# Performance work log

Measured on AMD Instinct MI355X. Metric: run time of the kernel, lower is better.

## Reference

```python
import jax, jax.numpy as jnp
import numpy as np

N, D, C, TOPK = 4096, 512, 512, 5


def setup_inputs() -> dict:
    key = jax.random.key(0)
    k1, k2, k3, k4 = jax.random.split(key, 4)
    feat1 = jax.random.normal(k1, (N, D), dtype=jnp.float32)
    feat2 = jax.random.normal(k2, (N, D), dtype=jnp.float32)
    # probs are softmax outputs in the original pipeline -> valid BCE inputs in (0,1)
    prob1 = jax.nn.softmax(jax.random.normal(k3, (N, C), dtype=jnp.float32), axis=-1)
    prob2 = jax.nn.softmax(jax.random.normal(k4, (N, C), dtype=jnp.float32), axis=-1)
    return {"feat1": feat1, "feat2": feat2, "prob1": prob1, "prob2": prob2, "topk": TOPK}


def reference(feat1, feat2, prob1, prob2, topk):
    # rank statistics on detached feat1: top-k feature indices, sorted as a set
    rank_idx = jnp.argsort(-feat1, axis=1)           # descending argsort, (N, D)
    top = jnp.sort(rank_idx[:, :topk], axis=1)       # (N, K) sorted top-k index sets
    # pair_enum layout: pair k = j*N + i with x1 -> row i (fast), x2 -> row j (slow).
    # Build the equivalent (N, N) matrices with rows=j, cols=i.
    rank_diff = jnp.abs(top[None, :, :] - top[:, None, :]).sum(-1)  # (N, N)
    target = (rank_diff == 0).astype(prob1.dtype)
    # pred_sim[k] = dot(prob1[i], prob2[j])  ->  P[j, i]
    pred_sim = prob2 @ prob1.T                        # (N, N)
    # BCELoss with torch's log clamp at -100
    log_p = jnp.clip(jnp.log(pred_sim), -100.0)
    log_1mp = jnp.clip(jnp.log(1.0 - pred_sim), -100.0)
    loss = -jnp.mean(target * log_p + (1.0 - target) * log_1mp)
    return loss
```

## Files before the change

### kernel.cpp

```cpp
#include <hip/hip_runtime.h>
#include <hip/hip_bf16.h>
#include <stdint.h>

#define NROWS 4096
#define CDIM  512
#define TOPK  5
#define BM    256
#define BK    32
#define NKT   16

typedef __bf16 bf16x8 __attribute__((ext_vector_type(8)));
typedef float  f32x4  __attribute__((ext_vector_type(4)));

__global__ void convert_kernel(const float* __restrict__ p1,
                               const float* __restrict__ p2,
                               __bf16* __restrict__ o1,
                               __bf16* __restrict__ o2) {
  const int t = blockIdx.x * 256 + threadIdx.x;
  const float* src;
  __bf16* dst;
  int e = t;
  if (t >= 262144) { src = p2; dst = o2; e = t - 262144; }
  else             { src = p1; dst = o1; }
  const int row   = e >> 6;
  const int k8    = e & 63;
  const int chunk = k8 >> 2;
  const int slot  = k8 & 3;
  const int dslot = slot ^ (row & 3);
  const float4 a = *(const float4*)(src + (size_t)row * CDIM + k8 * 8);
  const float4 b = *(const float4*)(src + (size_t)row * CDIM + k8 * 8 + 4);
  bf16x8 v;
  v[0]=(__bf16)a.x; v[1]=(__bf16)a.y; v[2]=(__bf16)a.z; v[3]=(__bf16)a.w;
  v[4]=(__bf16)b.x; v[5]=(__bf16)b.y; v[6]=(__bf16)b.z; v[7]=(__bf16)b.w;
  *(bf16x8*)(dst + (size_t)row * CDIM + chunk * 32 + dslot * 8) = v;
}

__global__ void topk_keys_kernel(const float* __restrict__ feat1,
                                 unsigned long long* __restrict__ keys) {
  const int row = blockIdx.x;
  const int l   = threadIdx.x;
  const float* r = feat1 + (size_t)row * CDIM;
  float v[8];
  const float4 a = *(const float4*)(r + l * 8);
  const float4 b = *(const float4*)(r + l * 8 + 4);
  v[0]=a.x; v[1]=a.y; v[2]=a.z; v[3]=a.w;
  v[4]=b.x; v[5]=b.y; v[6]=b.z; v[7]=b.w;

  int sel[TOPK];
#pragma unroll
  for (int s = 0; s < TOPK; ++s) {
    float bv = -__builtin_inff();
    int   bi = 0x7fffffff;
#pragma unroll
    for (int t = 0; t < 8; ++t) {
      if (v[t] > bv) { bv = v[t]; bi = l * 8 + t; }
    }
#pragma unroll
    for (int off = 32; off > 0; off >>= 1) {
      float ov = __shfl_xor(bv, off);
      int   oi = __shfl_xor(bi, off);
      if (ov > bv || (ov == bv && oi < bi)) { bv = ov; bi = oi; }
    }
    sel[s] = bi;
    const int loc = bi - l * 8;
    if (loc >= 0 && loc < 8) v[loc] = -__builtin_inff();
  }

#define CSWAP(x, y) { int mn = min(sel[x], sel[y]); int mx = max(sel[x], sel[y]); sel[x] = mn; sel[y] = mx; }
  CSWAP(0,1) CSWAP(3,4) CSWAP(2,4) CSWAP(2,3) CSWAP(1,4)
  CSWAP(0,3) CSWAP(0,2) CSWAP(1,3) CSWAP(1,2)
#undef CSWAP

  if (l == 0) {
    unsigned long long key =
        (unsigned long long)sel[0]
      | ((unsigned long long)sel[1] << 9)
      | ((unsigned long long)sel[2] << 18)
      | ((unsigned long long)sel[3] << 27)
      | ((unsigned long long)sel[4] << 36);
    keys[row] = key;
  }
}

__global__ __launch_bounds__(512, 2) void
gemm_loss_kernel(const __bf16* __restrict__ p1b,
                 const __bf16* __restrict__ p2b,
                 const unsigned long long* __restrict__ keys,
                 float* __restrict__ partials) {
  __shared__ __bf16 sm[4][2][BM * BK];
  __shared__ float  red[512];

  const int tid = threadIdx.x;
  const int l   = tid & 63, w = tid >> 6;
  const int wr  = w >> 2,  wc = w & 3;
  const int lr  = l & 15,  kq = l >> 4;

  const int bid = blockIdx.x;
  const int x   = bid & 7, wv = bid >> 3;
  const int it  = (x & 3) * 4 + (wv & 3);
  const int jt  = (x >> 2) * 8 + (wv >> 2);
  const int ib  = it * BM, jb = jt * BM;

  f32x4 acc[8][4] = {};

  auto stage = [&](int slot, int kt) {
    const int k0 = kt * BK;
#pragma unroll
    for (int i = 0; i < 2; ++i) {
      const int c   = i * 512 + tid;
      const int row = c >> 2;
      const int ps  = c & 3;
      const __bf16* gA = p2b + (size_t)(jb + row) * CDIM + k0 + ps * 8;
      const __bf16* gB = p1b + (size_t)(ib + row) * CDIM + k0 + ps * 8;
      __bf16* lA = &sm[slot][0][(i * 512 + w * 64) * 8];
      __bf16* lB = &sm[slot][1][(i * 512 + w * 64) * 8];
      __builtin_amdgcn_global_load_lds(
          (const __attribute__((address_space(1))) unsigned int*)(const void*)gA,
          (__attribute__((address_space(3))) unsigned int*)(void*)lA, 16, 0, 0);
      __builtin_amdgcn_global_load_lds(
          (const __attribute__((address_space(1))) unsigned int*)(const void*)gB,
          (__attribute__((address_space(3))) unsigned int*)(void*)lB, 16, 0, 0);
    }
  };

  auto compute = [&](int slot) {
    bf16x8 af[8], bfr[4];
#pragma unroll
    for (int n = 0; n < 4; ++n) {
      const int r  = wc * 64 + n * 16 + lr;
      const int ps = kq ^ (r & 3);
      bfr[n] = *(const bf16x8*)&sm[slot][1][r * 32 + ps * 8];
    }
#pragma unroll
    for (int m = 0; m < 8; ++m) {
      const int r  = wr * 128 + m * 16 + lr;
      const int ps = kq ^ (r & 3);
      af[m] = *(const bf16x8*)&sm[slot][0][r * 32 + ps * 8];
    }
    __builtin_amdgcn_s_setprio(1);
#pragma unroll
    for (int m = 0; m < 8; ++m)
#pragma unroll
      for (int n = 0; n < 4; ++n)
        acc[m][n] = __builtin_amdgcn_mfma_f32_16x16x32_bf16(af[m], bfr[n], acc[m][n], 0, 0, 0);
    __builtin_amdgcn_s_setprio(0);
  };

  stage(0, 0);
  stage(1, 1);

  for (int kt = 0; kt < NKT - 2; ++kt) {
    stage((kt + 2) & 3, kt + 2);
    asm volatile("s_waitcnt vmcnt(8)" ::: "memory");
    __builtin_amdgcn_s_barrier();
    __builtin_amdgcn_sched_barrier(0);
    compute(kt & 3);
  }
  asm volatile("s_waitcnt vmcnt(4)" ::: "memory");
  __builtin_amdgcn_s_barrier();
  __builtin_amdgcn_sched_barrier(0);
  compute((NKT - 2) & 3);
  asm volatile("s_waitcnt vmcnt(0)" ::: "memory");
  __builtin_amdgcn_s_barrier();
  __builtin_amdgcn_sched_barrier(0);
  compute((NKT - 1) & 3);

  unsigned long long kj[32], ki[4];
#pragma unroll
  for (int m = 0; m < 8; ++m)
#pragma unroll
    for (int r = 0; r < 4; ++r)
      kj[m * 4 + r] = keys[jb + wr * 128 + m * 16 + kq * 4 + r];
#pragma unroll
  for (int n = 0; n < 4; ++n)
    ki[n] = keys[ib + wc * 64 + n * 16 + lr];

  float sum = 0.f;
#pragma unroll
  for (int m = 0; m < 8; ++m)
#pragma unroll
    for (int n = 0; n < 4; ++n)
#pragma unroll
      for (int r = 0; r < 4; ++r) {
        const float p = acc[m][n][r];
        const bool  t = (kj[m * 4 + r] == ki[n]);
        const float xx = t ? p : (1.0f - p);
        sum += fmaxf(__logf(xx), -100.0f);
      }

  red[tid] = sum;
  __syncthreads();
#pragma unroll
  for (int s = 256; s > 0; s >>= 1) {
    if (tid < s) red[tid] += red[tid + s];
    __syncthreads();
  }
  if (tid == 0) partials[bid] = red[0];
}

__global__ void finalize_kernel(const float* __restrict__ partials,
                                float* __restrict__ out) {
  __shared__ float red[256];
  red[threadIdx.x] = partials[threadIdx.x];
  __syncthreads();
  for (int st = 128; st > 0; st >>= 1) {
    if (threadIdx.x < st) red[threadIdx.x] += red[threadIdx.x + st];
    __syncthreads();
  }
  if (threadIdx.x == 0) out[0] = -red[0] * (1.0f / 16777216.0f);
}

extern "C" void kernel_launch(void* const* d_in, const int* in_sizes, int n_in,
                              void* d_out, int out_size, void* d_ws, size_t ws_size,
                              hipStream_t stream) {
  (void)in_sizes; (void)n_in; (void)out_size; (void)ws_size;
  const float* feat1 = (const float*)d_in[0];
  const float* prob1 = (const float*)d_in[2];
  const float* prob2 = (const float*)d_in[3];

  __bf16* o1 = (__bf16*)d_ws;
  __bf16* o2 = (__bf16*)((char*)d_ws + (size_t)NROWS * CDIM * 2);
  unsigned long long* keys = (unsigned long long*)((char*)d_ws + (size_t)NROWS * CDIM * 4);
  float* partials = (float*)((char*)d_ws + (size_t)NROWS * CDIM * 4 + NROWS * 8);

  convert_kernel<<<2048, 256, 0, stream>>>(prob1, prob2, o1, o2);
  topk_keys_kernel<<<NROWS, 64, 0, stream>>>(feat1, keys);
  gemm_loss_kernel<<<256, 512, 0, stream>>>(o1, o2, keys, partials);
  finalize_kernel<<<1, 256, 0, stream>>>(partials, (float*)d_out);
}
```

Before: 45.37 us.

## Fuse prep kernels, k-major bf16 layout, smaller GEMM tiles with triple buffering

Merges the bf16 conversion and top-k key kernels into a single prep launch. The converted operands are written in a k-tile-major layout, so each GEMM stage becomes one contiguous block load. The GEMM tile shrinks from 256x256 to 128x256, which doubles the grid to 512 blocks, and uses a 3-slot LDS ring with launch bounds raised to 4 blocks/CU. This targets better CU occupancy and fewer launches, at the cost of more operand re-reads per output element and less latency hiding with shallower buffering.

```diff
diff --git a/kernel.cpp b/kernel.cpp
--- a/kernel.cpp
+++ b/kernel.cpp
@@ -5,89 +5,82 @@
 #define NROWS 4096
 #define CDIM  512
 #define TOPK  5
-#define BM    256
+#define BMJ   128
+#define BNI   256
 #define BK    32
 #define NKT   16
 
 typedef __bf16 bf16x8 __attribute__((ext_vector_type(8)));
 typedef float  f32x4  __attribute__((ext_vector_type(4)));
-
-__global__ void convert_kernel(const float* __restrict__ p1,
-                               const float* __restrict__ p2,
-                               __bf16* __restrict__ o1,
-                               __bf16* __restrict__ o2) {
-  const int t = blockIdx.x * 256 + threadIdx.x;
-  const float* src;
-  __bf16* dst;
-  int e = t;
-  if (t >= 262144) { src = p2; dst = o2; e = t - 262144; }
-  else             { src = p1; dst = o1; }
-  const int row   = e >> 6;
-  const int k8    = e & 63;
-  const int chunk = k8 >> 2;
-  const int slot  = k8 & 3;
-  const int dslot = slot ^ (row & 3);
-  const float4 a = *(const float4*)(src + (size_t)row * CDIM + k8 * 8);
-  const float4 b = *(const float4*)(src + (size_t)row * CDIM + k8 * 8 + 4);
-  bf16x8 v;
-  v[0]=(__bf16)a.x; v[1]=(__bf16)a.y; v[2]=(__bf16)a.z; v[3]=(__bf16)a.w;
-  v[4]=(__bf16)b.x; v[5]=(__bf16)b.y; v[6]=(__bf16)b.z; v[7]=(__bf16)b.w;
-  *(bf16x8*)(dst + (size_t)row * CDIM + chunk * 32 + dslot * 8) = v;
-}
-
-__global__ void topk_keys_kernel(const float* __restrict__ feat1,
-                                 unsigned long long* __restrict__ keys) {
-  const int row = blockIdx.x;
-  const int l   = threadIdx.x;
-  const float* r = feat1 + (size_t)row * CDIM;
-  float v[8];
-  const float4 a = *(const float4*)(r + l * 8);
-  const float4 b = *(const float4*)(r + l * 8 + 4);
-  v[0]=a.x; v[1]=a.y; v[2]=a.z; v[3]=a.w;
-  v[4]=b.x; v[5]=b.y; v[6]=b.z; v[7]=b.w;
-
-  int sel[TOPK];
-#pragma unroll
-  for (int s = 0; s < TOPK; ++s) {
-    float bv = -__builtin_inff();
-    int   bi = 0x7fffffff;
-#pragma unroll
-    for (int t = 0; t < 8; ++t) {
-      if (v[t] > bv) { bv = v[t]; bi = l * 8 + t; }
-    }
-#pragma unroll
-    for (int off = 32; off > 0; off >>= 1) {
-      float ov = __shfl_xor(bv, off);
-      int   oi = __shfl_xor(bi, off);
-      if (ov > bv || (ov == bv && oi < bi)) { bv = ov; bi = oi; }
-    }
-    sel[s] = bi;
-    const int loc = bi - l * 8;
-    if (loc >= 0 && loc < 8) v[loc] = -__builtin_inff();
-  }
-
+typedef unsigned long long u64;
+
+__global__ __launch_bounds__(256) void
+prep_kernel(const float* __restrict__ p1, const float* __restrict__ p2,
+            const float* __restrict__ feat1,
+            __bf16* __restrict__ o1, __bf16* __restrict__ o2,
+            u64* __restrict__ keys) {
+  const int bid = blockIdx.x, tid = threadIdx.x;
+  if (bid < 2048) {
+    const int arr = bid >> 10;
+    const int b2  = bid & 1023;
+    const int kt  = b2 >> 6;
+    const int c   = (b2 & 63) * 256 + tid;
+    const int row = c >> 2;
+    const int s   = c & 3;
+    const float* src = (arr ? p2 : p1) + (size_t)row * CDIM + kt * 32 + s * 8;
+    __bf16*      dst = (arr ? o2 : o1) + ((size_t)kt * NROWS + row) * 32 + ((s ^ (row & 3)) * 8);
+    const float4 a = *(const float4*)src;
+    const float4 b = *(const float4*)(src + 4);
+    bf16x8 v;
+    v[0]=(__bf16)a.x; v[1]=(__bf16)a.y; v[2]=(__bf16)a.z; v[3]=(__bf16)a.w;
+    v[4]=(__bf16)b.x; v[5]=(__bf16)b.y; v[6]=(__bf16)b.z; v[7]=(__bf16)b.w;
+    *(bf16x8*)dst = v;
+  } else {
+    const int row = (bid - 2048) * 4 + (tid >> 6);
+    const int l   = tid & 63;
+    const float* r = feat1 + (size_t)row * CDIM;
+    float v[8];
+    const float4 a = *(const float4*)(r + l * 8);
+    const float4 b = *(const float4*)(r + l * 8 + 4);
+    v[0]=a.x; v[1]=a.y; v[2]=a.z; v[3]=a.w;
+    v[4]=b.x; v[5]=b.y; v[6]=b.z; v[7]=b.w;
+
+    int sel[TOPK];
+#pragma unroll
+    for (int s = 0; s < TOPK; ++s) {
+      float bv = -__builtin_inff();
+      int   bi = 0x7fffffff;
+#pragma unroll
+      for (int t = 0; t < 8; ++t)
+        if (v[t] > bv) { bv = v[t]; bi = l * 8 + t; }
+#pragma unroll
+      for (int off = 32; off > 0; off >>= 1) {
+        float ov = __shfl_xor(bv, off);
+        int   oi = __shfl_xor(bi, off);
+        if (ov > bv || (ov == bv && oi < bi)) { bv = ov; bi = oi; }
+      }
+      sel[s] = bi;
+      const int loc = bi - l * 8;
+      if (loc >= 0 && loc < 8) v[loc] = -__builtin_inff();
+    }
 #define CSWAP(x, y) { int mn = min(sel[x], sel[y]); int mx = max(sel[x], sel[y]); sel[x] = mn; sel[y] = mx; }
-  CSWAP(0,1) CSWAP(3,4) CSWAP(2,4) CSWAP(2,3) CSWAP(1,4)
-  CSWAP(0,3) CSWAP(0,2) CSWAP(1,3) CSWAP(1,2)
+    CSWAP(0,1) CSWAP(3,4) CSWAP(2,4) CSWAP(2,3) CSWAP(1,4)
+    CSWAP(0,3) CSWAP(0,2) CSWAP(1,3) CSWAP(1,2)
 #undef CSWAP
-
-  if (l == 0) {
-    unsigned long long key =
-        (unsigned long long)sel[0]
-      | ((unsigned long long)sel[1] << 9)
-      | ((unsigned long long)sel[2] << 18)
-      | ((unsigned long long)sel[3] << 27)
-      | ((unsigned long long)sel[4] << 36);
-    keys[row] = key;
-  }
-}
-
-__global__ __launch_bounds__(512, 2) void
-gemm_loss_kernel(const __bf16* __restrict__ p1b,
-                 const __bf16* __restrict__ p2b,
-                 const unsigned long long* __restrict__ keys,
+    if (l == 0) {
+      keys[row] = (u64)sel[0] | ((u64)sel[1] << 9) | ((u64)sel[2] << 18)
+                | ((u64)sel[3] << 27) | ((u64)sel[4] << 36);
+    }
+  }
+}
+
+__global__ __launch_bounds__(512, 4) void
+gemm_loss_kernel(const __bf16* __restrict__ o1k,
+                 const __bf16* __restrict__ o2k,
+                 const u64* __restrict__ keys,
                  float* __restrict__ partials) {
-  __shared__ __bf16 sm[4][2][BM * BK];
+  __shared__ __bf16 smA[3][BMJ * BK];
+  __shared__ __bf16 smB[3][BNI * BK];
   __shared__ float  red[512];
 
   const int tid = threadIdx.x;
@@ -96,50 +89,46 @@
   const int lr  = l & 15,  kq = l >> 4;
 
   const int bid = blockIdx.x;
-  const int x   = bid & 7, wv = bid >> 3;
-  const int it  = (x & 3) * 4 + (wv & 3);
-  const int jt  = (x >> 2) * 8 + (wv >> 2);
-  const int ib  = it * BM, jb = jt * BM;
-
-  f32x4 acc[8][4] = {};
+  const int x   = bid & 7, v = bid >> 3;
+  const int jt  = (x & 3) * 8 + (v & 7);
+  const int it  = (x >> 2) * 8 + (v >> 3);
+  const int jb  = jt * BMJ, ib = it * BNI;
+
+  f32x4 acc[4][4] = {};
+
+  const __bf16* gA0 = o2k + (size_t)jb * 32;
+  const __bf16* gB0 = o1k + (size_t)ib * 32;
 
   auto stage = [&](int slot, int kt) {
-    const int k0 = kt * BK;
+    const size_t ko = (size_t)kt * NROWS * 32;
+    __builtin_amdgcn_global_load_lds(
+        (const __attribute__((address_space(1))) unsigned int*)(const void*)(gA0 + ko + tid * 8),
+        (__attribute__((address_space(3))) unsigned int*)(void*)&smA[slot][w * 512], 16, 0, 0);
 #pragma unroll
     for (int i = 0; i < 2; ++i) {
-      const int c   = i * 512 + tid;
-      const int row = c >> 2;
-      const int ps  = c & 3;
-      const __bf16* gA = p2b + (size_t)(jb + row) * CDIM + k0 + ps * 8;
-      const __bf16* gB = p1b + (size_t)(ib + row) * CDIM + k0 + ps * 8;
-      __bf16* lA = &sm[slot][0][(i * 512 + w * 64) * 8];
-      __bf16* lB = &sm[slot][1][(i * 512 + w * 64) * 8];
       __builtin_amdgcn_global_load_lds(
-          (const __attribute__((address_space(1))) unsigned int*)(const void*)gA,
-          (__attribute__((address_space(3))) unsigned int*)(void*)lA, 16, 0, 0);
-      __builtin_amdgcn_global_load_lds(
-          (const __attribute__((address_space(1))) unsigned int*)(const void*)gB,
-          (__attribute__((address_space(3))) unsigned int*)(void*)lB, 16, 0, 0);
+          (const __attribute__((address_space(1))) unsigned int*)(const void*)(gB0 + ko + (i * 512 + tid) * 8),
+          (__attribute__((address_space(3))) unsigned int*)(void*)&smB[slot][i * 4096 + w * 512], 16, 0, 0);
     }
   };
 
   auto compute = [&](int slot) {
-    bf16x8 af[8], bfr[4];
+    bf16x8 af[4], bfr[4];
+#pragma unroll
+    for (int m = 0; m < 4; ++m) {
+      const int r = wr * 64 + m * 16 + lr;
+      const int p = kq ^ (r & 3);
+      af[m] = *(const bf16x8*)&smA[slot][r * 32 + p * 8];
+    }
 #pragma unroll
     for (int n = 0; n < 4; ++n) {
-      const int r  = wc * 64 + n * 16 + lr;
-      const int ps = kq ^ (r & 3);
-      bfr[n] = *(const bf16x8*)&sm[slot][1][r * 32 + ps * 8];
-    }
-#pragma unroll
-    for (int m = 0; m < 8; ++m) {
-      const int r  = wr * 128 + m * 16 + lr;
-      const int ps = kq ^ (r & 3);
-      af[m] = *(const bf16x8*)&sm[slot][0][r * 32 + ps * 8];
+      const int r = wc * 64 + n * 16 + lr;
+      const int p = kq ^ (r & 3);
+      bfr[n] = *(const bf16x8*)&smB[slot][r * 32 + p * 8];
     }
     __builtin_amdgcn_s_setprio(1);
 #pragma unroll
-    for (int m = 0; m < 8; ++m)
+    for (int m = 0; m < 4; ++m)
 #pragma unroll
       for (int n = 0; n < 4; ++n)
         acc[m][n] = __builtin_amdgcn_mfma_f32_16x16x32_bf16(af[m], bfr[n], acc[m][n], 0, 0, 0);
@@ -148,45 +137,34 @@
 
   stage(0, 0);
   stage(1, 1);
-
-  for (int kt = 0; kt < NKT - 2; ++kt) {
-    stage((kt + 2) & 3, kt + 2);
-    asm volatile("s_waitcnt vmcnt(8)" ::: "memory");
+  for (int kt = 0; kt < NKT; ++kt) {
+    if (kt == NKT - 1) asm volatile("s_waitcnt vmcnt(0)" ::: "memory");
+    else               asm volatile("s_waitcnt vmcnt(3)" ::: "memory");
     __builtin_amdgcn_s_barrier();
     __builtin_amdgcn_sched_barrier(0);
-    compute(kt & 3);
-  }
-  asm volatile("s_waitcnt vmcnt(4)" ::: "memory");
-  __builtin_amdgcn_s_barrier();
-  __builtin_amdgcn_sched_barrier(0);
-  compute((NKT - 2) & 3);
-  asm volatile("s_waitcnt vmcnt(0)" ::: "memory");
-  __builtin_amdgcn_s_barrier();
-  __builtin_amdgcn_sched_barrier(0);
-  compute((NKT - 1) & 3);
-
-  unsigned long long kj[32], ki[4];
-#pragma unroll
-  for (int m = 0; m < 8; ++m)
-#pragma unroll
-    for (int r = 0; r < 4; ++r)
-      kj[m * 4 + r] = keys[jb + wr * 128 + m * 16 + kq * 4 + r];
+    if (kt + 2 < NKT) stage((kt + 2) % 3, kt + 2);
+    compute(kt % 3);
+  }
+
+  u64 ki[4];
 #pragma unroll
   for (int n = 0; n < 4; ++n)
     ki[n] = keys[ib + wc * 64 + n * 16 + lr];
 
   float sum = 0.f;
 #pragma unroll
-  for (int m = 0; m < 8; ++m)
-#pragma unroll
-    for (int n = 0; n < 4; ++n)
-#pragma unroll
-      for (int r = 0; r < 4; ++r) {
+  for (int m = 0; m < 4; ++m)
+#pragma unroll
+    for (int r = 0; r < 4; ++r) {
+      const u64 kj = keys[jb + wr * 64 + m * 16 + kq * 4 + r];
+#pragma unroll
+      for (int n = 0; n < 4; ++n) {
         const float p = acc[m][n][r];
-        const bool  t = (kj[m * 4 + r] == ki[n]);
+        const bool  t = (kj == ki[n]);
         const float xx = t ? p : (1.0f - p);
         sum += fmaxf(__logf(xx), -100.0f);
       }
+    }
 
   red[tid] = sum;
   __syncthreads();
@@ -201,7 +179,7 @@
 __global__ void finalize_kernel(const float* __restrict__ partials,
                                 float* __restrict__ out) {
   __shared__ float red[256];
-  red[threadIdx.x] = partials[threadIdx.x];
+  red[threadIdx.x] = partials[threadIdx.x] + partials[threadIdx.x + 256];
   __syncthreads();
   for (int st = 128; st > 0; st >>= 1) {
     if (threadIdx.x < st) red[threadIdx.x] += red[threadIdx.x + st];
@@ -220,11 +198,10 @@
 
   __bf16* o1 = (__bf16*)d_ws;
   __bf16* o2 = (__bf16*)((char*)d_ws + (size_t)NROWS * CDIM * 2);
-  unsigned long long* keys = (unsigned long long*)((char*)d_ws + (size_t)NROWS * CDIM * 4);
+  u64*   keys = (u64*)((char*)d_ws + (size_t)NROWS * CDIM * 4);
   float* partials = (float*)((char*)d_ws + (size_t)NROWS * CDIM * 4 + NROWS * 8);
 
-  convert_kernel<<<2048, 256, 0, stream>>>(prob1, prob2, o1, o2);
-  topk_keys_kernel<<<NROWS, 64, 0, stream>>>(feat1, keys);
-  gemm_loss_kernel<<<256, 512, 0, stream>>>(o1, o2, keys, partials);
+  prep_kernel<<<3072, 256, 0, stream>>>(prob1, prob2, feat1, o1, o2, keys);
+  gemm_loss_kernel<<<512, 512, 0, stream>>>(o1, o2, keys, partials);
   finalize_kernel<<<1, 256, 0, stream>>>(partials, (float*)d_out);
 }
```

Result: faster. 40.13 us (-11.5%).
